# Kernel tuning notes

Hardware: AMD Instinct MI355X
Metric: run time of the kernel (lower is better)

## Reference

```python
import jax, jax.numpy as jnp
import numpy as np

N_HEAD = 16
NEG = 1e10


def setup_inputs() -> dict:
    key = jax.random.key(0)
    k1, k2, k3 = jax.random.split(key, 3)
    nx = 1024
    B, S = 2, 2048
    x = jax.random.normal(k1, (B, S, nx), dtype=jnp.float32)
    w_attn = jax.random.normal(k2, (nx, 3 * nx), dtype=jnp.float32) * (1.0 / np.sqrt(nx))
    b_attn = jnp.zeros((3 * nx,), dtype=jnp.float32)
    w_proj = jax.random.normal(k3, (nx, nx), dtype=jnp.float32) * (1.0 / np.sqrt(nx))
    b_proj = jnp.zeros((nx,), dtype=jnp.float32)
    return {"x": x, "w_attn": w_attn, "b_attn": b_attn, "w_proj": w_proj, "b_proj": b_proj}


def reference(x, w_attn, b_attn, w_proj, b_proj):
    B, S, nx = x.shape
    d = nx // N_HEAD
    qkv = x @ w_attn + b_attn                      # [B,S,3*nx]
    q, k, v = jnp.split(qkv, 3, axis=-1)
    # split heads: [B,S,nx] -> [B,H,S,d]
    q = q.reshape(B, S, N_HEAD, d).transpose(0, 2, 1, 3)
    k = k.reshape(B, S, N_HEAD, d).transpose(0, 2, 1, 3)
    v = v.reshape(B, S, N_HEAD, d).transpose(0, 2, 1, 3)
    # present: stack of (key stored as [B,H,S,d], value) like torch code
    present = jnp.stack((k, v))                    # [2,B,H,S,d]
    # scores with scale and additive causal mask (GPT-2 style: w*b - 1e10*(1-b))
    w = jnp.einsum('bhqd,bhkd->bhqk', q, k) / jnp.sqrt(jnp.float32(d))
    mask = jnp.tril(jnp.ones((S, S), dtype=w.dtype))[None, None]
    w = w * mask - NEG * (1.0 - mask)
    w = jax.nn.softmax(w, axis=-1)
    a = jnp.einsum('bhqk,bhkd->bhqd', w, v)        # [B,H,S,d]
    a = a.transpose(0, 2, 1, 3).reshape(B, S, nx)  # merge heads
    a = a @ w_proj + b_proj
    return (a, present)
```

## Files before the change

### kernel.cpp

```cpp
#include <hip/hip_runtime.h>
#include <stdint.h>
#include <stddef.h>

#define DEVI __device__ __forceinline__

typedef __bf16 bf16x8 __attribute__((ext_vector_type(8)));
typedef float  f32x4  __attribute__((ext_vector_type(4)));
typedef float  f32x16 __attribute__((ext_vector_type(16)));
typedef unsigned short u16;
typedef uint32_t u32;
typedef u16 u16x8 __attribute__((ext_vector_type(8)));
typedef u16 u16x4 __attribute__((ext_vector_type(4)));
typedef u32 u32x2 __attribute__((ext_vector_type(2)));
typedef u32 u32x4 __attribute__((ext_vector_type(4)));

typedef __attribute__((address_space(1))) void as1_void;
typedef __attribute__((address_space(3))) void as3_void;

static constexpr float SC = 0.18033688011112042f;

DEVI u16 f2bf(float f) {
  uint32_t u = __builtin_bit_cast(uint32_t, f);
  u += 0x7fffu + ((u >> 16) & 1u);
  return (u16)(u >> 16);
}

DEVI void gload_lds16(const void* g, void* l) {
  __builtin_amdgcn_global_load_lds((as1_void*)(void*)g, (as3_void*)l, 16, 0, 0);
}

#if __has_builtin(__builtin_amdgcn_exp2f)
DEVI float fast_exp2(float x) { return __builtin_amdgcn_exp2f(x); }
#else
DEVI float fast_exp2(float x) { return exp2f(x); }
#endif

DEVI u32 cvtpk(float lo, float hi) {
  u32 r;
  asm("v_cvt_pk_bf16_f32 %0, %1, %2" : "=v"(r) : "v"(lo), "v"(hi));
  return r;
}
DEVI void plswap(u32& a, u32& b) {
  asm("v_permlane32_swap_b32 %0, %1" : "+v"(a), "+v"(b));
}

__global__ __launch_bounds__(256) void k_cvt(const float* __restrict__ in,
                                             u16* __restrict__ out, int n) {
  int i = (blockIdx.x * 256 + threadIdx.x) * 4;
  if (i >= n) return;
  const float4 v = *(const float4*)(in + i);
  u16x4 o = { f2bf(v.x), f2bf(v.y), f2bf(v.z), f2bf(v.w) };
  *(u16x4*)(out + i) = o;
}

__global__ __launch_bounds__(256) void k_tcvt(const float* __restrict__ in,
                                              u16* __restrict__ out, int R, int C) {
  __shared__ float tile[32][33];
  const int c0 = blockIdx.x * 32, r0 = blockIdx.y * 32;
  const int tx = threadIdx.x, ty = threadIdx.y;
#pragma unroll
  for (int i = ty; i < 32; i += 8)
    tile[i][tx] = in[(size_t)(r0 + i) * C + (c0 + tx)];
  __syncthreads();
#pragma unroll
  for (int i = ty; i < 32; i += 8)
    out[(size_t)(c0 + i) * R + (r0 + tx)] = f2bf(tile[tx][i]);
}

__global__ __launch_bounds__(256) void k_vt(const u16* __restrict__ in,
                                            u16* __restrict__ out) {
  __shared__ u16 tile[64][72];
  const int tid = threadIdx.x;
  const int s0 = blockIdx.x * 64;
  const int bh = blockIdx.y;
  const size_t ib = (size_t)bh * 131072;
#pragma unroll
  for (int it = 0; it < 2; ++it) {
    const int r = (tid >> 3) + it * 32;
    const int c8 = (tid & 7) * 8;
    u16x8 v = *(const u16x8*)(in + ib + (size_t)(s0 + r) * 64 + c8);
    *(u16x8*)&tile[r][c8] = v;
  }
  __syncthreads();
#pragma unroll
  for (int it = 0; it < 2; ++it) {
    const int d = (tid >> 3) + it * 32;
    const int s8 = (tid & 7) * 8;
    u16x8 v;
#pragma unroll
    for (int jj = 0; jj < 8; ++jj) v[jj] = tile[s8 + jj][d];
    *(u16x8*)(out + ib + (size_t)d * 2048 + s0 + s8) = v;
  }
}

template <int EPI>
__global__ __launch_bounds__(256) void k_gemm(
    const u16* __restrict__ A, const u16* __restrict__ Bt,
    const float* __restrict__ bias,
    u16* __restrict__ wq, u16* __restrict__ wk, u16* __restrict__ wv,
    float* __restrict__ pk, float* __restrict__ pv, float* __restrict__ of) {
  constexpr int K = 1024;
  constexpr int NT = K / 32;
  __shared__ __align__(16) u16 Ash[3][128 * 32];
  __shared__ __align__(16) u16 Bsh[3][128 * 32];
  const int tid = threadIdx.x;
  const int lane = tid & 63, wid = tid >> 6;
  const int wm = wid >> 1, wn = wid & 1;
  const int lr = lane & 15, lg = lane >> 4;

  const int nwgx = gridDim.x;
  const int nwg = nwgx * gridDim.y;
  int lbid = blockIdx.y * nwgx + blockIdx.x;
  lbid = (lbid & 7) * (nwg >> 3) + (lbid >> 3);
  const int m0 = (lbid / nwgx) * 128, n0 = (lbid % nwgx) * 128;

  const int c = wid * 64 + lane;
  const int sw = (((c & 3) ^ ((c >> 3) & 3)) * 8);
  const u16* Ag1 = A + (size_t)(m0 + (c >> 2)) * K + sw;
  const u16* Ag2 = A + (size_t)(m0 + 64 + (c >> 2)) * K + sw;
  const u16* Bg1 = Bt + (size_t)(n0 + (c >> 2)) * K + sw;
  const u16* Bg2 = Bt + (size_t)(n0 + 64 + (c >> 2)) * K + sw;

  f32x4 acc[4][4];
#pragma unroll
  for (int i = 0; i < 4; ++i)
#pragma unroll
    for (int j = 0; j < 4; ++j) acc[i][j] = (f32x4)0.0f;

#define STAGE(sel, kk)                                        \
  {                                                           \
    gload_lds16(Ag1 + (kk), &Ash[sel][wid * 512]);            \
    gload_lds16(Ag2 + (kk), &Ash[sel][2048 + wid * 512]);     \
    gload_lds16(Bg1 + (kk), &Bsh[sel][wid * 512]);            \
    gload_lds16(Bg2 + (kk), &Bsh[sel][2048 + wid * 512]);     \
  }

  STAGE(0, 0)
  STAGE(1, 32)
  asm volatile("s_waitcnt vmcnt(4)" ::: "memory");
  __builtin_amdgcn_sched_barrier(0);
  __builtin_amdgcn_s_barrier();
  __builtin_amdgcn_sched_barrier(0);

  const int xg = (lr >> 1) & 3;

  int cur = 0;
  for (int j = 0; j < NT; ++j) {
    const bool pf = (j + 2 < NT);
    int nb = cur + 2; if (nb >= 3) nb -= 3;
    if (pf) STAGE(nb, (j + 2) * 32)
    bf16x8 af[4], bfr[4];
#pragma unroll
    for (int f = 0; f < 4; ++f) {
      af[f]  = *(const bf16x8*)&Ash[cur][(wm * 64 + f * 16 + lr) * 32 + ((lg ^ xg) * 8)];
      bfr[f] = *(const bf16x8*)&Bsh[cur][(wn * 64 + f * 16 + lr) * 32 + ((lg ^ xg) * 8)];
    }
    __builtin_amdgcn_s_setprio(1);
#pragma unroll
    for (int i = 0; i < 4; ++i)
#pragma unroll
      for (int jj = 0; jj < 4; ++jj)
        acc[i][jj] = __builtin_amdgcn_mfma_f32_16x16x32_bf16(af[i], bfr[jj], acc[i][jj], 0, 0, 0);
    __builtin_amdgcn_s_setprio(0);
    if (pf) asm volatile("s_waitcnt vmcnt(4)" ::: "memory");
    else    asm volatile("s_waitcnt vmcnt(0)" ::: "memory");
    __builtin_amdgcn_sched_barrier(0);
    __builtin_amdgcn_s_barrier();
    __builtin_amdgcn_sched_barrier(0);
    cur = (cur + 1 == 3) ? 0 : cur + 1;
  }
#undef STAGE

  if constexpr (EPI == 0) {
#pragma unroll
    for (int j = 0; j < 4; ++j) {
      const int n = n0 + wn * 64 + j * 16 + lr;
      const float bv = bias[n];
      const int sec = n >> 10;
      const int nn = n & 1023;
      const int h = nn >> 6, dd = nn & 63;
#pragma unroll
      for (int i = 0; i < 4; ++i) {
        const int mb = m0 + wm * 64 + i * 16 + lg * 4;
        const int bb = mb >> 11, ss = mb & 2047;
        const size_t ib = (size_t)(bb * 16 + h) * 131072 + (size_t)ss * 64 + dd;
        if (sec == 0) {
#pragma unroll
          for (int r = 0; r < 4; ++r)
            wq[ib + (size_t)r * 64] = f2bf(acc[i][j][r] + bv);
        } else if (sec == 1) {
#pragma unroll
          for (int r = 0; r < 4; ++r) {
            const float v = acc[i][j][r] + bv;
            wk[ib + (size_t)r * 64] = f2bf(v);
            pk[ib + (size_t)r * 64] = v;
          }
        } else {
#pragma unroll
          for (int r = 0; r < 4; ++r) {
            const float v = acc[i][j][r] + bv;
            wv[ib + (size_t)r * 64] = f2bf(v);
            pv[ib + (size_t)r * 64] = v;
          }
        }
      }
    }
  } else {
#pragma unroll
    for (int j = 0; j < 4; ++j) {
      const int n = n0 + wn * 64 + j * 16 + lr;
      const float bv = bias[n];
#pragma unroll
      for (int i = 0; i < 4; ++i) {
        const int mb = m0 + wm * 64 + i * 16 + lg * 4;
#pragma unroll
        for (int r = 0; r < 4; ++r)
          of[(size_t)(mb + r) * 1024 + n] = acc[i][j][r] + bv;
      }
    }
  }
}

__global__ __launch_bounds__(128, 2) void k_attn(const u16* __restrict__ Q,
                                                 const u16* __restrict__ Kp,
                                                 const u16* __restrict__ VT,
                                                 u16* __restrict__ AO) {
  __shared__ __align__(16) u16 Ksh[2][2][4096];

  const int tid = threadIdx.x;
  const int lane = tid & 63, w = tid >> 6;
  const int l31 = lane & 31, hi = lane >> 5;
  const int bid = blockIdx.x;
  const int bh = bid & 31;
  const int p = bid >> 5;
  const int b = bh >> 4, h = bh & 15;
  const size_t hb = (size_t)bh * (2048 * 64);
  const int xr = l31 & 7;

  const u16* Kg = Kp + hb + (size_t)(lane >> 3) * 64 + (size_t)(((lane & 7) ^ (lane >> 3)) * 8);
  const u16* Vg = VT + hb + (size_t)l31 * 2048 + hi * 8;

  float* OslB = (float*)&Ksh[0][0][0];
  float* ML   = (float*)&Ksh[0][1][0];

#define STAGEK(sel, jt)                                       \
  {                                                           \
    u16* kd = &Ksh[w][sel][0];                                \
    const u16* ks = Kg + (size_t)(jt) * 4096;                 \
    gload_lds16(ks,        kd);                               \
    gload_lds16(ks +  512, kd +  512);                        \
    gload_lds16(ks + 1024, kd + 1024);                        \
    gload_lds16(ks + 1536, kd + 1536);                        \
    gload_lds16(ks + 2048, kd + 2048);                        \
    gload_lds16(ks + 2560, kd + 2560);                        \
    gload_lds16(ks + 3072, kd + 3072);                        \
    gload_lds16(ks + 3584, kd + 3584);                        \
  }

#define GL16(dst, ptr, IMM)                                           \
  asm volatile("global_load_dwordx4 %0, %1, off offset:" #IMM         \
               : "=v"(dst) : "v"(ptr));

#define LOADV(jt)                                             \
  {                                                           \
    const u16* vp0 = Vg + (size_t)(jt) * 64;                  \
    const u16* vp1 = vp0 + 65536;                             \
    GL16(vv[0][0], vp0, 0)  GL16(vv[0][1], vp0, 32)           \
    GL16(vv[0][2], vp0, 64) GL16(vv[0][3], vp0, 96)           \
    GL16(vv[1][0], vp1, 0)  GL16(vv[1][1], vp1, 32)           \
    GL16(vv[1][2], vp1, 64) GL16(vv[1][3], vp1, 96)           \
  }

  for (int t = 0; t < 2; ++t) {
    const int qtl = t ? (63 - p) : p;
    const int T = (qtl >> 1) + 1;
    const int mid = (T + 1) >> 1;
    const int lo  = w ? mid : 0;
    const int hiE = w ? T : mid;
    const int qb = qtl * 32;

    const u16* Qp2 = Q + hb + (size_t)(qb + l31) * 64 + hi * 8;
    const bf16x8 qf0 = *(const bf16x8*)(Qp2);
    const bf16x8 qf1 = *(const bf16x8*)(Qp2 + 16);
    const bf16x8 qf2 = *(const bf16x8*)(Qp2 + 32);
    const bf16x8 qf3 = *(const bf16x8*)(Qp2 + 48);

    f32x16 o0 = (f32x16)0.0f, o1 = (f32x16)0.0f;
    float mrun = -1e30f, lrun = 0.0f;

    if (lo < hiE) {
      STAGEK(0, lo)
      int cur = 0;
      for (int jt = lo; jt < hiE; ++jt) {
        const bool hn = (jt + 1 < hiE);
        u32x4 vv[2][4];
        LOADV(jt)
        if (hn) STAGEK(cur ^ 1, jt + 1)
        if (hn) asm volatile("s_waitcnt vmcnt(16)" ::: "memory");
        else    asm volatile("s_waitcnt vmcnt(8)"  ::: "memory");
        __builtin_amdgcn_sched_barrier(0);

        const u16* Kb = &Ksh[w][cur][0];
        bf16x8 kf[2][4];
#pragma unroll
        for (int s = 0; s < 2; ++s)
#pragma unroll
          for (int c = 0; c < 4; ++c)
            kf[s][c] = *(const bf16x8*)&Kb[(s * 32 + l31) * 64 + (((2 * c + hi) ^ xr) * 8)];

        f32x16 s0 = (f32x16)0.0f, s1 = (f32x16)0.0f;
        __builtin_amdgcn_s_setprio(1);
        s0 = __builtin_amdgcn_mfma_f32_32x32x16_bf16(kf[0][0], qf0, s0, 0, 0, 0);
        s1 = __builtin_amdgcn_mfma_f32_32x32x16_bf16(kf[1][0], qf0, s1, 0, 0, 0);
        s0 = __builtin_amdgcn_mfma_f32_32x32x16_bf16(kf[0][1], qf1, s0, 0, 0, 0);
        s1 = __builtin_amdgcn_mfma_f32_32x32x16_bf16(kf[1][1], qf1, s1, 0, 0, 0);
        s0 = __builtin_amdgcn_mfma_f32_32x32x16_bf16(kf[0][2], qf2, s0, 0, 0, 0);
        s1 = __builtin_amdgcn_mfma_f32_32x32x16_bf16(kf[1][2], qf2, s1, 0, 0, 0);
        s0 = __builtin_amdgcn_mfma_f32_32x32x16_bf16(kf[0][3], qf3, s0, 0, 0, 0);
        s1 = __builtin_amdgcn_mfma_f32_32x32x16_bf16(kf[1][3], qf3, s1, 0, 0, 0);
        __builtin_amdgcn_s_setprio(0);

        if (jt == T - 1) {
          const int qrel = (qtl & 1) * 32 + l31;
          const int h4 = hi * 4;
#pragma unroll
          for (int r = 0; r < 16; ++r) {
            const int kp = (r & 3) + ((r >> 2) << 3) + h4;
            s0[r] = (kp <= qrel) ? s0[r] : -1e30f;
            s1[r] = (kp + 32 <= qrel) ? s1[r] : -1e30f;
          }
        }

        float t8[8];
#pragma unroll
        for (int r = 0; r < 8; ++r)
          t8[r] = fmaxf(fmaxf(s0[r], s0[r + 8]), fmaxf(s1[r], s1[r + 8]));
        float tm = fmaxf(fmaxf(fmaxf(t8[0], t8[1]), fmaxf(t8[2], t8[3])),
                         fmaxf(fmaxf(t8[4], t8[5]), fmaxf(t8[6], t8[7])));
        tm = fmaxf(tm, __shfl_xor(tm, 32));
        if (!__all(tm <= mrun)) {
          const float mnew = fmaxf(mrun, tm);
          const float al = fast_exp2((mrun - mnew) * SC);
          mrun = mnew;
          lrun *= al;
#pragma unroll
          for (int r = 0; r < 16; ++r) { o0[r] *= al; o1[r] *= al; }
        }
        const float nb2 = -mrun * SC;
#pragma unroll
        for (int r = 0; r < 16; ++r) {
          s0[r] = fast_exp2(fmaf(s0[r], SC, nb2));
          s1[r] = fast_exp2(fmaf(s1[r], SC, nb2));
        }
        float u8[8];
#pragma unroll
        for (int r = 0; r < 8; ++r)
          u8[r] = (s0[r] + s0[r + 8]) + (s1[r] + s1[r + 8]);
        lrun += ((u8[0] + u8[1]) + (u8[2] + u8[3])) + ((u8[4] + u8[5]) + (u8[6] + u8[7]));

        bf16x8 pb0, pb1, pb2, pb3;
#define PACK_CHUNK(sv, bb, dst)                                   \
        {                                                         \
          u32 a0 = cvtpk(sv[bb + 0], sv[bb + 1]);                 \
          u32 a1 = cvtpk(sv[bb + 2], sv[bb + 3]);                 \
          u32 a2 = cvtpk(sv[bb + 4], sv[bb + 5]);                 \
          u32 a3 = cvtpk(sv[bb + 6], sv[bb + 7]);                 \
          plswap(a0, a2);                                         \
          plswap(a1, a3);                                         \
          u32x4 fv = {a0, a1, a2, a3};                            \
          dst = __builtin_bit_cast(bf16x8, fv);                   \
        }
        PACK_CHUNK(s0, 0, pb0)
        PACK_CHUNK(s0, 8, pb1)
        PACK_CHUNK(s1, 0, pb2)
        PACK_CHUNK(s1, 8, pb3)
#undef PACK_CHUNK

        if (hn) asm volatile("s_waitcnt vmcnt(8)" ::: "memory");
        else    asm volatile("s_waitcnt vmcnt(0)" ::: "memory");
        __builtin_amdgcn_sched_barrier(0);

        const bf16x8 vf00 = __builtin_bit_cast(bf16x8, vv[0][0]);
        const bf16x8 vf01 = __builtin_bit_cast(bf16x8, vv[0][1]);
        const bf16x8 vf02 = __builtin_bit_cast(bf16x8, vv[0][2]);
        const bf16x8 vf03 = __builtin_bit_cast(bf16x8, vv[0][3]);
        const bf16x8 vf10 = __builtin_bit_cast(bf16x8, vv[1][0]);
        const bf16x8 vf11 = __builtin_bit_cast(bf16x8, vv[1][1]);
        const bf16x8 vf12 = __builtin_bit_cast(bf16x8, vv[1][2]);
        const bf16x8 vf13 = __builtin_bit_cast(bf16x8, vv[1][3]);

        __builtin_amdgcn_s_setprio(1);
        o0 = __builtin_amdgcn_mfma_f32_32x32x16_bf16(vf00, pb0, o0, 0, 0, 0);
        o1 = __builtin_amdgcn_mfma_f32_32x32x16_bf16(vf10, pb0, o1, 0, 0, 0);
        o0 = __builtin_amdgcn_mfma_f32_32x32x16_bf16(vf01, pb1, o0, 0, 0, 0);
        o1 = __builtin_amdgcn_mfma_f32_32x32x16_bf16(vf11, pb1, o1, 0, 0, 0);
        o0 = __builtin_amdgcn_mfma_f32_32x32x16_bf16(vf02, pb2, o0, 0, 0, 0);
        o1 = __builtin_amdgcn_mfma_f32_32x32x16_bf16(vf12, pb2, o1, 0, 0, 0);
        o0 = __builtin_amdgcn_mfma_f32_32x32x16_bf16(vf03, pb3, o0, 0, 0, 0);
        o1 = __builtin_amdgcn_mfma_f32_32x32x16_bf16(vf13, pb3, o1, 0, 0, 0);
        __builtin_amdgcn_s_setprio(0);

        cur ^= 1;
      }
    }

    __syncthreads();
    if (w == 1) {
#pragma unroll
      for (int r = 0; r < 16; ++r) {
        OslB[r * 64 + lane]        = o0[r];
        OslB[(16 + r) * 64 + lane] = o1[r];
      }
      ML[lane]      = mrun;
      ML[64 + lane] = lrun;
    }
    __syncthreads();
    if (w == 0) {
      const float mB = ML[lane];
      const float lB = ML[64 + lane];
      const float m  = fmaxf(mrun, mB);
      const float al = fast_exp2((mrun - m) * SC);
      const float bt = fast_exp2((mB - m) * SC);
      lrun = lrun * al + lB * bt;
#pragma unroll
      for (int r = 0; r < 16; ++r) {
        o0[r] = o0[r] * al + OslB[r * 64 + lane] * bt;
        o1[r] = o1[r] * al + OslB[(16 + r) * 64 + lane] * bt;
      }

      const float lt = lrun + __shfl_xor(lrun, 32);
      const float inv = 1.0f / lt;
      u16* aorow = AO + (size_t)(b * 2048 + qb + l31) * 1024 + h * 64 + hi * 4;
#pragma unroll
      for (int g2 = 0; g2 < 4; ++g2) {
        u32 w0s = cvtpk(o0[4 * g2 + 0] * inv, o0[4 * g2 + 1] * inv);
        u32 w1s = cvtpk(o0[4 * g2 + 2] * inv, o0[4 * g2 + 3] * inv);
        u32x2 ww = {w0s, w1s};
        *(u32x2*)(aorow + g2 * 8) = ww;
      }
#pragma unroll
      for (int g2 = 0; g2 < 4; ++g2) {
        u32 w0s = cvtpk(o1[4 * g2 + 0] * inv, o1[4 * g2 + 1] * inv);
        u32 w1s = cvtpk(o1[4 * g2 + 2] * inv, o1[4 * g2 + 3] * inv);
        u32x2 ww = {w0s, w1s};
        *(u32x2*)(aorow + 32 + g2 * 8) = ww;
      }
      asm volatile("s_waitcnt lgkmcnt(0)" ::: "memory");
      __builtin_amdgcn_sched_barrier(0);
    }
  }
#undef STAGEK
#undef LOADV
#undef GL16
}

extern "C" void kernel_launch(void* const* d_in, const int* in_sizes, int n_in,
                              void* d_out, int out_size, void* d_ws, size_t ws_size,
                              hipStream_t stream) {
  const float* x      = (const float*)d_in[0];
  const float* w_attn = (const float*)d_in[1];
  const float* b_attn = (const float*)d_in[2];
  const float* w_proj = (const float*)d_in[3];
  const float* b_proj = (const float*)d_in[4];
  float* out = (float*)d_out;

  char* ws = (char*)d_ws;
  u16* x_bf  = (u16*)(ws);
  u16* wat_t = (u16*)(ws + 8388608);
  u16* wpj_t = (u16*)(ws + 14680064);
  u16* q_ws  = (u16*)(ws + 16777216);
  u16* k_ws  = (u16*)(ws + 25165824);
  u16* v_ws  = (u16*)(ws + 33554432);
  u16* a_ws  = (u16*)(ws + 41943040);
  u16* vT_ws = (u16*)(ws);

  k_cvt<<<4096, 256, 0, stream>>>(x, x_bf, 4194304);
  k_tcvt<<<dim3(96, 32), dim3(32, 8), 0, stream>>>(w_attn, wat_t, 1024, 3072);
  k_tcvt<<<dim3(32, 32), dim3(32, 8), 0, stream>>>(w_proj, wpj_t, 1024, 1024);

  k_gemm<0><<<dim3(24, 32), 256, 0, stream>>>(x_bf, wat_t, b_attn,
                                              q_ws, k_ws, v_ws,
                                              out + 4194304, out + 8388608, nullptr);

  k_vt<<<dim3(32, 32), 256, 0, stream>>>(v_ws, vT_ws);

  k_attn<<<dim3(1024), 128, 0, stream>>>(q_ws, k_ws, vT_ws, a_ws);

  k_gemm<1><<<dim3(8, 32), 256, 0, stream>>>(a_ws, wpj_t, b_proj,
                                             nullptr, nullptr, nullptr,
                                             nullptr, nullptr, out);
}
```

Baseline: 132.2 us.

## Move present K/V fp32 writes out of QKV GEMM epilogue; remap tiles per XCD

The QKV GEMM epilogue now writes only bf16 Q/K/V. The fp32 `present` tensors are rebuilt afterwards from the bf16 copies, by a new coalesced widening kernel and inside the V-transpose kernel. The goal is to remove the scattered fp32 stores from the GEMM epilogue. The GEMM block-to-tile mapping is also changed so that each XCD owns a contiguous range of N columns, for better L2 locality. The trade-offs are that `present` now holds bf16-rounded values, and that the present-V region is written twice (by k_present and k_vt), adding memory traffic.

```diff
diff --git a/kernel.cpp b/kernel.cpp
--- a/kernel.cpp
+++ b/kernel.cpp
@@ -25,6 +25,10 @@
   return (u16)(u >> 16);
 }
 
+DEVI float bf2f(u16 v) {
+  return __builtin_bit_cast(float, (u32)v << 16);
+}
+
 DEVI void gload_lds16(const void* g, void* l) {
   __builtin_amdgcn_global_load_lds((as1_void*)(void*)g, (as3_void*)l, 16, 0, 0);
 }
@@ -53,6 +57,17 @@
   *(u16x4*)(out + i) = o;
 }
 
+__global__ __launch_bounds__(256) void k_present(const u16* __restrict__ in,
+                                                 float* __restrict__ out, int n) {
+  int i = (blockIdx.x * 256 + threadIdx.x) * 8;
+  if (i >= n) return;
+  u16x8 v = *(const u16x8*)(in + i);
+  float4 a = { bf2f(v[0]), bf2f(v[1]), bf2f(v[2]), bf2f(v[3]) };
+  float4 b = { bf2f(v[4]), bf2f(v[5]), bf2f(v[6]), bf2f(v[7]) };
+  *(float4*)(out + i) = a;
+  *(float4*)(out + i + 4) = b;
+}
+
 __global__ __launch_bounds__(256) void k_tcvt(const float* __restrict__ in,
                                               u16* __restrict__ out, int R, int C) {
   __shared__ float tile[32][33];
@@ -68,7 +83,8 @@
 }
 
 __global__ __launch_bounds__(256) void k_vt(const u16* __restrict__ in,
-                                            u16* __restrict__ out) {
+                                            u16* __restrict__ out,
+                                            float* __restrict__ pv) {
   __shared__ u16 tile[64][72];
   const int tid = threadIdx.x;
   const int s0 = blockIdx.x * 64;
@@ -80,6 +96,10 @@
     const int c8 = (tid & 7) * 8;
     u16x8 v = *(const u16x8*)(in + ib + (size_t)(s0 + r) * 64 + c8);
     *(u16x8*)&tile[r][c8] = v;
+    float4 f0 = { bf2f(v[0]), bf2f(v[1]), bf2f(v[2]), bf2f(v[3]) };
+    float4 f1 = { bf2f(v[4]), bf2f(v[5]), bf2f(v[6]), bf2f(v[7]) };
+    *(float4*)(pv + ib + (size_t)(s0 + r) * 64 + c8) = f0;
+    *(float4*)(pv + ib + (size_t)(s0 + r) * 64 + c8 + 4) = f1;
   }
   __syncthreads();
 #pragma unroll
@@ -98,7 +118,7 @@
     const u16* __restrict__ A, const u16* __restrict__ Bt,
     const float* __restrict__ bias,
     u16* __restrict__ wq, u16* __restrict__ wk, u16* __restrict__ wv,
-    float* __restrict__ pk, float* __restrict__ pv, float* __restrict__ of) {
+    float* __restrict__ of) {
   constexpr int K = 1024;
   constexpr int NT = K / 32;
   __shared__ __align__(16) u16 Ash[3][128 * 32];
@@ -109,10 +129,12 @@
   const int lr = lane & 15, lg = lane >> 4;
 
   const int nwgx = gridDim.x;
-  const int nwg = nwgx * gridDim.y;
-  int lbid = blockIdx.y * nwgx + blockIdx.x;
-  lbid = (lbid & 7) * (nwg >> 3) + (lbid >> 3);
-  const int m0 = (lbid / nwgx) * 128, n0 = (lbid % nwgx) * 128;
+  const int npx = nwgx >> 3;
+  const int orig = blockIdx.y * nwgx + blockIdx.x;
+  const int xcd = orig & 7;
+  const int idx = orig >> 3;
+  const int n0 = (xcd * npx + idx % npx) * 128;
+  const int m0 = (idx / npx) * 128;
 
   const int c = wid * 64 + lane;
   const int sw = (((c & 3) ^ ((c >> 3) & 3)) * 8);
@@ -184,25 +206,10 @@
         const int mb = m0 + wm * 64 + i * 16 + lg * 4;
         const int bb = mb >> 11, ss = mb & 2047;
         const size_t ib = (size_t)(bb * 16 + h) * 131072 + (size_t)ss * 64 + dd;
-        if (sec == 0) {
-#pragma unroll
-          for (int r = 0; r < 4; ++r)
-            wq[ib + (size_t)r * 64] = f2bf(acc[i][j][r] + bv);
-        } else if (sec == 1) {
-#pragma unroll
-          for (int r = 0; r < 4; ++r) {
-            const float v = acc[i][j][r] + bv;
-            wk[ib + (size_t)r * 64] = f2bf(v);
-            pk[ib + (size_t)r * 64] = v;
-          }
-        } else {
-#pragma unroll
-          for (int r = 0; r < 4; ++r) {
-            const float v = acc[i][j][r] + bv;
-            wv[ib + (size_t)r * 64] = f2bf(v);
-            pv[ib + (size_t)r * 64] = v;
-          }
-        }
+        u16* dst = (sec == 0) ? wq : (sec == 1) ? wk : wv;
+#pragma unroll
+        for (int r = 0; r < 4; ++r)
+          dst[ib + (size_t)r * 64] = f2bf(acc[i][j][r] + bv);
       }
     }
   } else {
@@ -479,14 +486,13 @@
   k_tcvt<<<dim3(32, 32), dim3(32, 8), 0, stream>>>(w_proj, wpj_t, 1024, 1024);
 
   k_gemm<0><<<dim3(24, 32), 256, 0, stream>>>(x_bf, wat_t, b_attn,
-                                              q_ws, k_ws, v_ws,
-                                              out + 4194304, out + 8388608, nullptr);
-
-  k_vt<<<dim3(32, 32), 256, 0, stream>>>(v_ws, vT_ws);
+                                              q_ws, k_ws, v_ws, nullptr);
+
+  k_present<<<4096, 256, 0, stream>>>(k_ws, out + 4194304, 8388608);
+  k_vt<<<dim3(32, 32), 256, 0, stream>>>(v_ws, vT_ws, out + 8388608);
 
   k_attn<<<dim3(1024), 128, 0, stream>>>(q_ws, k_ws, vT_ws, a_ws);
 
   k_gemm<1><<<dim3(8, 32), 256, 0, stream>>>(a_ws, wpj_t, b_proj,
-                                             nullptr, nullptr, nullptr,
-                                             nullptr, nullptr, out);
-}
+                                             nullptr, nullptr, nullptr, out);
+}
```

Measured after the change: 141.3 us. +6.9%, slower.
